# Kernel tuning notes

Measured on AMD Instinct MI355X. Metric: run time of the kernel, lower is better.

The kernel has to match this reference:

```python
import jax, jax.numpy as jnp
import numpy as np

B, S, H, HEADS, STEP = 128, 256, 128, 8, 1


def setup_inputs() -> dict:
    key = jax.random.key(0)
    ks = jax.random.split(key, 20)
    rn = lambda k, shape: jax.random.normal(k, shape, dtype=jnp.float32) * 0.1
    return {
        "A": jax.random.uniform(ks[0], (B, S, 2 * S), dtype=jnp.float32),
        "hidden": jax.random.normal(ks[1], (B, S, H), dtype=jnp.float32),
        "mask": jnp.ones((B, S), dtype=jnp.int32),
        "w_ih": rn(ks[2], (3 * H, 2 * H)),
        "w_hh": rn(ks[3], (3 * H, H)),
        "b_ih": rn(ks[4], (3 * H,)),
        "b_hh": rn(ks[5], (3 * H,)),
        "b_iah": rn(ks[6], (H,)),
        "b_oah": rn(ks[7], (H,)),
        "W_ein": rn(ks[8], (H, H)), "b_ein": rn(ks[9], (H,)),
        "W_eout": rn(ks[10], (H, H)), "b_eout": rn(ks[11], (H,)),
        "W_q0": rn(ks[12], (H, H)), "b_q0": rn(ks[13], (H,)),
        "W_q1": rn(ks[14], (H, H)), "b_q1": rn(ks[15], (H,)),
        "W_q2": rn(ks[16], (H, H)), "b_q2": rn(ks[17], (H,)),
    }


def _forward(A, hidden, mask, w_ih, w_hh, b_ih, b_hh, b_iah, b_oah,
             W_ein, b_ein, W_eout, b_eout, W_q0, b_q0, W_q1, b_q1, W_q2, b_q2):
    b, s, h = hidden.shape
    dk = h // HEADS
    # ---- GNN: gated graph propagation (GRU cell over adjacency messages) ----
    for _ in range(STEP):
        msg_in = A[:, :, :s] @ (hidden @ W_ein.T + b_ein) + b_iah    # [B,S,H]
        msg_out = A[:, :, s:] @ (hidden @ W_eout.T + b_eout) + b_oah  # [B,S,H]
        inputs = jnp.concatenate([msg_in, msg_out], axis=2)           # [B,S,2H]
        gi = inputs @ w_ih.T + b_ih                                   # [B,S,3H]
        gh = hidden @ w_hh.T + b_hh                                   # [B,S,3H]
        i_r, i_i, i_n = jnp.split(gi, 3, axis=2)
        h_r, h_i, h_n = jnp.split(gh, 3, axis=2)
        resetgate = jax.nn.sigmoid(i_r + h_r)
        inputgate = jax.nn.sigmoid(i_i + h_i)
        newgate = jnp.tanh(i_n + resetgate * h_n)
        hidden = hidden - inputgate * (hidden - newgate)
    # ---- query: hidden state of the last valid item in each session ----
    last_idx = jnp.sum(mask, axis=1) - 1
    ht1 = hidden[jnp.arange(b), last_idx]                             # [B,H]
    # ---- LastAttenion: sigmoid score + double softmax readout ----
    q0 = (ht1 @ W_q0.T + b_q0).reshape(b, HEADS, dk)                  # [B,h,dk]
    q1 = (hidden @ W_q1.T + b_q1).reshape(b, s, HEADS, dk).transpose(0, 2, 1, 3)
    q2 = (hidden @ W_q2.T + b_q2).reshape(b, s, HEADS, dk).transpose(0, 2, 1, 3)
    # q0 is expanded over the query axis, so every score row is identical
    alpha = jax.nn.sigmoid(jnp.einsum('bhd,bhjd->bhj', q0, q1))        # [B,h,S]
    alpha = jnp.broadcast_to(alpha[:, :, None, :], (b, HEADS, s, s))   # [B,h,S,S]
    alpha = jax.nn.softmax(alpha, axis=-1)
    row_keep = (mask > 0)[:, None, :, None]                            # [B,1,S,1]
    alpha = jnp.where(row_keep, alpha, -jnp.inf)
    alpha = jax.nn.softmax(2.0 * alpha, axis=1)                        # over heads
    alpha = jnp.where(row_keep, alpha, 0.0)  # guard fully-masked rows (torch would NaN)
    x = jnp.einsum('bhij,bhjd->bhid', alpha, q2)                       # [B,h,S,dk]
    x = x.transpose(0, 2, 1, 3).reshape(b, s, h)                       # [B,S,H]
    a = jnp.sum(x * mask[:, :, None].astype(x.dtype), axis=1)          # [B,H]
    return a


def reference(A, hidden, mask, w_ih, w_hh, b_ih, b_hh, b_iah, b_oah,
              W_ein, b_ein, W_eout, b_eout, W_q0, b_q0, W_q1, b_q1, W_q2, b_q2):
    return _forward(A, hidden, mask, w_ih, w_hh, b_ih, b_hh, b_iah, b_oah,
                    W_ein, b_ein, W_eout, b_eout, W_q0, b_q0, W_q1, b_q1, W_q2, b_q2)
```

## Files before the change

kernel.cpp:

```cpp
#include <hip/hip_runtime.h>
#include <cstdint>
#include <cstddef>

#define BB   128
#define SS   256
#define HH   128
#define NH   8
#define DKK  16

typedef unsigned short u16;
typedef __attribute__((ext_vector_type(8))) short   sh8;
typedef __attribute__((ext_vector_type(4))) float   f32x4;

__device__ __forceinline__ float sigmoidf_(float x) { return 1.f / (1.f + expf(-x)); }

__device__ __forceinline__ u16 f2bf(float x) {
    union { float f; unsigned int u; } v; v.f = x;
    unsigned int r = (v.u + 0x7fffu + ((v.u >> 16) & 1u)) >> 16;
    return (u16)r;
}
__device__ __forceinline__ float bf2f(u16 u) {
    union { unsigned int u; float f; } v; v.u = ((unsigned int)u) << 16;
    return v.f;
}
__device__ __forceinline__ float bflo(unsigned u) {
    union { unsigned u; float f; } v; v.u = u << 16; return v.f;
}
__device__ __forceinline__ float bfhi(unsigned u) {
    union { unsigned u; float f; } v; v.u = u & 0xffff0000u; return v.f;
}

#define BKk 32
#define PK  40

template<int XMODE, int OMODE>
__global__ __launch_bounds__(256) void gemm_mfma(
    const void* __restrict__ Xa, const void* __restrict__ Xc, int ldx, int ldx1, int ksplit,
    long long sXb, long long sXh,
    const u16* __restrict__ Bw, int ldb, long long sBb, long long sBh,
    const float* __restrict__ bias,
    void* __restrict__ Out, long long ldo, long long sOb, long long sOh,
    int K, const u16* __restrict__ hid)
{
    __shared__ __align__(16) char smem[2 * 128 * PK * 2];
    u16* As = (u16*)smem;
    u16* Bs = (u16*)(smem + 128 * PK * 2);

    const int t  = threadIdx.x;
    const int bm = blockIdx.x * 128;
    const int bn = blockIdx.y * 128;
    const long long zb = blockIdx.z >> 1, zh = blockIdx.z & 1;

    const u16* Bp = Bw + zb * sBb + zh * sBh;

    const int wave = t >> 6, lane = t & 63;
    const int wr = (wave >> 1) * 64, wc = (wave & 1) * 64;
    const int fm = lane & 15, fq = lane >> 4;

    f32x4 acc[4][4] = {};

    const int r0  = t >> 2, kk0 = (t & 3) * 8;
    const int r1  = t >> 3, kk1 = (t & 7) * 4;

    uint4  px0, px1, pb0, pb1;
    float4 pf0, pf1, pf2, pf3;

#define LOADX32(K0)                                                                  \
    if (XMODE == 1) {                                                                \
        const float* Xf_ = (const float*)Xa + zb * sXb + zh * sXh;                   \
        const float* xp_ = Xf_ + (long long)(bm + r1) * ldx + (K0) + kk1;            \
        pf0 = *(const float4*)(xp_);                                                 \
        pf1 = *(const float4*)(xp_ + 32LL * ldx);                                    \
        pf2 = *(const float4*)(xp_ + 64LL * ldx);                                    \
        pf3 = *(const float4*)(xp_ + 96LL * ldx);                                    \
    } else if (XMODE == 2 && (K0) >= ksplit) {                                       \
        const u16* xp_ = (const u16*)Xc + (long long)(bm + r0) * ldx1                \
                         + ((K0) - ksplit) + kk0;                                    \
        px0 = *(const uint4*)(xp_);                                                  \
        px1 = *(const uint4*)(xp_ + 64LL * ldx1);                                    \
    } else {                                                                         \
        const u16* xp_ = (const u16*)Xa + (long long)(bm + r0) * ldx + (K0) + kk0;   \
        px0 = *(const uint4*)(xp_);                                                  \
        px1 = *(const uint4*)(xp_ + 64LL * ldx);                                     \
    }

#define LOADB32(K0)                                                                  \
    {                                                                                \
        const u16* bp_ = Bp + (long long)(bn + r0) * ldb + (K0) + kk0;               \
        pb0 = *(const uint4*)(bp_);                                                  \
        pb1 = *(const uint4*)(bp_ + 64LL * ldb);                                     \
    }

    LOADX32(0)
    LOADB32(0)

    for (int k0 = 0; k0 < K; k0 += BKk) {
        if (XMODE == 1) {
            ushort4 w0 = { f2bf(pf0.x), f2bf(pf0.y), f2bf(pf0.z), f2bf(pf0.w) };
            ushort4 w1 = { f2bf(pf1.x), f2bf(pf1.y), f2bf(pf1.z), f2bf(pf1.w) };
            ushort4 w2 = { f2bf(pf2.x), f2bf(pf2.y), f2bf(pf2.z), f2bf(pf2.w) };
            ushort4 w3 = { f2bf(pf3.x), f2bf(pf3.y), f2bf(pf3.z), f2bf(pf3.w) };
            *(ushort4*)&As[(r1     ) * PK + kk1] = w0;
            *(ushort4*)&As[(r1 + 32) * PK + kk1] = w1;
            *(ushort4*)&As[(r1 + 64) * PK + kk1] = w2;
            *(ushort4*)&As[(r1 + 96) * PK + kk1] = w3;
        } else {
            *(uint4*)&As[(r0     ) * PK + kk0] = px0;
            *(uint4*)&As[(r0 + 64) * PK + kk0] = px1;
        }
        *(uint4*)&Bs[(r0     ) * PK + kk0] = pb0;
        *(uint4*)&Bs[(r0 + 64) * PK + kk0] = pb1;
        __syncthreads();

        if (k0 + BKk < K) {
            LOADX32(k0 + BKk)
            LOADB32(k0 + BKk)
        }

        sh8 af[4], bfr[4];
        #pragma unroll
        for (int i = 0; i < 4; i++) af[i]  = *(const sh8*)&As[(wr + i * 16 + fm) * PK + fq * 8];
        #pragma unroll
        for (int j = 0; j < 4; j++) bfr[j] = *(const sh8*)&Bs[(wc + j * 16 + fm) * PK + fq * 8];
        #pragma unroll
        for (int i = 0; i < 4; i++)
            #pragma unroll
            for (int j = 0; j < 4; j++)
                acc[i][j] = __builtin_amdgcn_mfma_f32_16x16x32_bf16(af[i], bfr[j], acc[i][j], 0, 0, 0);
        __syncthreads();
    }
#undef LOADX32
#undef LOADB32

    #pragma unroll
    for (int j = 0; j < 4; j++) {
        const int col = bn + wc + j * 16 + fm;
        const float bj = bias ? bias[col] : 0.f;
        #pragma unroll
        for (int i = 0; i < 4; i++) {
            const int row0 = bm + wr + i * 16 + fq * 4;
            if (OMODE == 1) {
                u16* O = (u16*)Out + zb * sOb + zh * sOh;
                #pragma unroll
                for (int r = 0; r < 4; r++)
                    O[(long long)(row0 + r) * ldo + col] = f2bf(acc[i][j][r] + bj);
            } else {
                u16* O = (u16*)Out + zb * sOb + zh * sOh;
                ushort4 w = { f2bf(acc[i][j][0] + bj), f2bf(acc[i][j][1] + bj),
                              f2bf(acc[i][j][2] + bj), f2bf(acc[i][j][3] + bj) };
                *(ushort4*)&O[(long long)col * ldo + row0] = w;
            }
        }
    }
}

#define BKD  64
#define PKB  72
#define ABUF (128 * PKB)
#define BUFH (2 * ABUF)

template<int XMODE, int OMODE>
__global__ __launch_bounds__(256) void gemm_dbuf(
    const void* __restrict__ Xa, const void* __restrict__ Xc, int ldx, int ldx1, int ksplit,
    long long sXb, long long sXh,
    const u16* __restrict__ Bw, int ldb, long long sBb, long long sBh,
    const float* __restrict__ bias,
    void* __restrict__ Out, long long ldo, long long sOb, long long sOh,
    int K, const u16* __restrict__ hid)
{
    __shared__ __align__(16) char smem[2 * BUFH * 2];
    u16* base = (u16*)smem;

    const int t  = threadIdx.x;
    const int bm = blockIdx.x * 128;
    const int bn = blockIdx.y * 128;
    const long long zb = blockIdx.z >> 1, zh = blockIdx.z & 1;

    const u16* Bp = Bw + zb * sBb + zh * sBh;

    const int wave = t >> 6, lane = t & 63;
    const int wr = (wave >> 1) * 64, wc = (wave & 1) * 64;
    const int fm = lane & 15, fq = lane >> 4;

    f32x4 acc[4][4] = {};

    const int rs = t >> 3, kcs = (t & 7) * 8;

    uint4  px0, px1, px2, px3, pb0, pb1, pb2, pb3;

#define LOADX64(K0)                                                                  \
    if (XMODE == 2 && (K0) >= ksplit) {                                              \
        const u16* xp_ = (const u16*)Xc + (long long)(bm + rs) * ldx1               \
                         + ((K0) - ksplit) + kcs;                                    \
        px0 = *(const uint4*)(xp_);                                                  \
        px1 = *(const uint4*)(xp_ + 32LL * ldx1);                                    \
        px2 = *(const uint4*)(xp_ + 64LL * ldx1);                                    \
        px3 = *(const uint4*)(xp_ + 96LL * ldx1);                                    \
    } else {                                                                         \
        const u16* xp_ = (const u16*)Xa + (long long)(bm + rs) * ldx + (K0) + kcs;   \
        px0 = *(const uint4*)(xp_);                                                  \
        px1 = *(const uint4*)(xp_ + 32LL * ldx);                                     \
        px2 = *(const uint4*)(xp_ + 64LL * ldx);                                     \
        px3 = *(const uint4*)(xp_ + 96LL * ldx);                                     \
    }

#define LOADB64(K0)                                                                  \
    {                                                                                \
        const u16* bp_ = Bp + (long long)(bn + rs) * ldb + (K0) + kcs;               \
        pb0 = *(const uint4*)(bp_);                                                  \
        pb1 = *(const uint4*)(bp_ + 32LL * ldb);                                     \
        pb2 = *(const uint4*)(bp_ + 64LL * ldb);                                     \
        pb3 = *(const uint4*)(bp_ + 96LL * ldb);                                     \
    }

#define COMMIT64(Ad, Bd)                                                             \
    *(uint4*)&(Ad)[(rs     ) * PKB + kcs] = px0;                                     \
    *(uint4*)&(Ad)[(rs + 32) * PKB + kcs] = px1;                                     \
    *(uint4*)&(Ad)[(rs + 64) * PKB + kcs] = px2;                                     \
    *(uint4*)&(Ad)[(rs + 96) * PKB + kcs] = px3;                                     \
    *(uint4*)&(Bd)[(rs     ) * PKB + kcs] = pb0;                                     \
    *(uint4*)&(Bd)[(rs + 32) * PKB + kcs] = pb1;                                     \
    *(uint4*)&(Bd)[(rs + 64) * PKB + kcs] = pb2;                                     \
    *(uint4*)&(Bd)[(rs + 96) * PKB + kcs] = pb3;

    const int nt = K / BKD;
    int cur = 0;

    LOADX64(0)
    LOADB64(0)
    {
        u16* Ad = base;
        u16* Bd = base + ABUF;
        COMMIT64(Ad, Bd)
    }
    __syncthreads();

    for (int tt = 0; tt < nt; ++tt) {
        if (tt + 1 < nt) {
            LOADX64((tt + 1) * BKD)
            LOADB64((tt + 1) * BKD)
        }

        const u16* Ac = base + cur * BUFH;
        const u16* Bc = Ac + ABUF;
        #pragma unroll
        for (int ks = 0; ks < 2; ks++) {
            sh8 af[4], bfr[4];
            #pragma unroll
            for (int i = 0; i < 4; i++)
                af[i]  = *(const sh8*)&Ac[(wr + i * 16 + fm) * PKB + ks * 32 + fq * 8];
            #pragma unroll
            for (int j = 0; j < 4; j++)
                bfr[j] = *(const sh8*)&Bc[(wc + j * 16 + fm) * PKB + ks * 32 + fq * 8];
            #pragma unroll
            for (int i = 0; i < 4; i++)
                #pragma unroll
                for (int j = 0; j < 4; j++)
                    acc[i][j] = __builtin_amdgcn_mfma_f32_16x16x32_bf16(af[i], bfr[j], acc[i][j], 0, 0, 0);
        }

        if (tt + 1 < nt) {
            u16* Ad = base + (cur ^ 1) * BUFH;
            u16* Bd = Ad + ABUF;
            COMMIT64(Ad, Bd)
        }
        __syncthreads();
        cur ^= 1;
    }
#undef LOADX64
#undef LOADB64
#undef COMMIT64

    {
        float* g4s = (float*)smem;
        const int chbase = bn >> 2;
        const int s_t = t >> 3;
        const int cq  = t & 7;
        u16* O = (u16*)Out;
        const int sbase = (wr ? 16 : 0) + fq * 4;
        #pragma unroll
        for (int i = 0; i < 4; i++) {
            #pragma unroll
            for (int j = 0; j < 4; j++) {
                const int q = wc + j * 16 + fm;
                const float bj = bias[bn + q];
                #pragma unroll
                for (int r = 0; r < 4; r++)
                    g4s[(sbase + r) * 132 + q] = acc[i][j][r] + bj;
            }
            __syncthreads();
            {
                const int grow = bm + i * 16 + (s_t < 16 ? s_t : s_t + 48);
                const ushort4 hv = *(const ushort4*)&hid[(long long)grow * HH + chbase + 4 * cq];
                const float hvv[4] = { bf2f(hv.x), bf2f(hv.y), bf2f(hv.z), bf2f(hv.w) };
                ushort4 w;
                u16* wp = (u16*)&w;
                #pragma unroll
                for (int m = 0; m < 4; m++) {
                    f32x4 gv = *(const f32x4*)&g4s[s_t * 132 + 16 * cq + 4 * m];
                    float rg = sigmoidf_(gv[0]);
                    float ig = sigmoidf_(gv[1]);
                    float ng = tanhf(gv[2] + rg * gv[3]);
                    wp[m] = f2bf(hvv[m] - ig * (hvv[m] - ng));
                }
                *(ushort4*)&O[(long long)grow * ldo + chbase + 4 * cq] = w;
            }
            __syncthreads();
        }
    }
}

__global__ __launch_bounds__(256) void k_prepw(
    const float* __restrict__ hidden, u16* __restrict__ h_bf,
    const float* __restrict__ w_ih, const float* __restrict__ w_hh,
    const float* __restrict__ b_ih, const float* __restrict__ b_hh,
    const float* __restrict__ b_iah, const float* __restrict__ b_oah,
    const float* __restrict__ W_ein, const float* __restrict__ b_ein,
    const float* __restrict__ W_eout, const float* __restrict__ b_eout,
    const float* __restrict__ W_q1, const float* __restrict__ b_q1,
    const float* __restrict__ W_q2, const float* __restrict__ b_q2,
    u16* __restrict__ W2bf, float* __restrict__ bias2,
    u16* __restrict__ Wcat, float* __restrict__ biascat,
    u16* __restrict__ Wq12, float* __restrict__ biasq12)
{
    int idx = blockIdx.x * 256 + threadIdx.x;
    {
        float4 v = ((const float4*)hidden)[idx];
        ushort4 w = { f2bf(v.x), f2bf(v.y), f2bf(v.z), f2bf(v.w) };
        ((ushort4*)h_bf)[idx] = w;
    }
    if (idx < 512 * 384) {
        int np = idx / 384, kk = idx % 384;
        int c = np >> 2, g = np & 3;
        float v;
        if (g < 2)       v = (kk < 256) ? w_ih[(g * 128 + c) * 256 + kk]
                                        : w_hh[(g * 128 + c) * 128 + kk - 256];
        else if (g == 2) v = (kk < 256) ? w_ih[(256 + c) * 256 + kk] : 0.f;
        else             v = (kk < 256) ? 0.f : w_hh[(256 + c) * 128 + kk - 256];
        W2bf[idx] = f2bf(v);
    }
    if (idx < 256 * 128) {
        int n = idx >> 7, k = idx & 127;
        Wcat[idx] = f2bf(n < 128 ? W_ein[n * 128 + k] : W_eout[(n - 128) * 128 + k]);
        Wq12[idx] = f2bf(n < 128 ? W_q1[n * 128 + k]  : W_q2[(n - 128) * 128 + k]);
    }
    if (idx < 512) {
        int np = idx, c = np >> 2, g = np & 3;
        float s;
        if (g < 2)       s = b_ih[g * 128 + c] + b_hh[g * 128 + c];
        else if (g == 2) s = b_ih[256 + c];
        else             s = b_hh[256 + c];
        if (g < 3) {
            int n = (g < 2) ? g * 128 + c : 256 + c;
            for (int k = 0; k < 128; k++)
                s += w_ih[n * 256 + k] * b_iah[k] + w_ih[n * 256 + 128 + k] * b_oah[k];
        }
        bias2[np] = s;
    }
    if (idx < 256) {
        biascat[idx] = idx < 128 ? b_ein[idx] : b_eout[idx - 128];
        biasq12[idx] = idx < 128 ? b_q1[idx]  : b_q2[idx - 128];
    }
}

__global__ __launch_bounds__(1024) void k_tail(
    const u16* __restrict__ hnew_bf, const int* __restrict__ mask,
    const u16* __restrict__ q12, const float* __restrict__ Wq0,
    const float* __restrict__ bq0, float* __restrict__ out)
{
    const int b = blockIdx.x, chb = blockIdx.y, t = threadIdx.x;
    __shared__ float red[1024];
    __shared__ float red2[1024][2];
    __shared__ float hs[HH];
    __shared__ float q0s[HH];
    __shared__ float p_s[NH][SS];
    __shared__ float w_s[NH][SS];
    __shared__ int s_nv;

    if (t < 256) {
        int v = mask[b * SS + t];
        #pragma unroll
        for (int m = 1; m < 64; m <<= 1) v += __shfl_xor(v, m, 64);
        if ((t & 63) == 0) red[t >> 6] = (float)v;
    }
    __syncthreads();
    if (t == 0) s_nv = (int)(red[0] + red[1] + red[2] + red[3]);
    __syncthreads();
    const int nv = s_nv;
    const int last = (nv - 1) & (SS - 1);

    if (t < HH) hs[t] = bf2f(hnew_bf[((size_t)b * SS + last) * HH + t]);
    __syncthreads();

    {
        const int n = t & 127, kh = t >> 7;
        const float* w = Wq0 + (size_t)n * HH + kh * 16;
        const float* h = hs + kh * 16;
        float s = 0.f;
        #pragma unroll
        for (int k = 0; k < 16; k++) s += h[k] * w[k];
        red[t] = s;
    }
    __syncthreads();
    if (t < HH) {
        float s = bq0[t];
        #pragma unroll
        for (int kh = 0; kh < 8; kh++) s += red[kh * 128 + t];
        q0s[t] = s;
    }
    __syncthreads();

    {
        const int j = t >> 2, q = t & 3;
        const u16* q1r = q12 + ((size_t)b * SS + j) * 256 + q * 32;
        uint4 va = *(const uint4*)(q1r);
        uint4 vb = *(const uint4*)(q1r + 8);
        uint4 vc = *(const uint4*)(q1r + 16);
        uint4 vd = *(const uint4*)(q1r + 24);
        const float* qa = q0s + q * 32;
        float s0 = qa[0]  * bflo(va.x) + qa[1]  * bfhi(va.x)
                 + qa[2]  * bflo(va.y) + qa[3]  * bfhi(va.y)
                 + qa[4]  * bflo(va.z) + qa[5]  * bfhi(va.z)
                 + qa[6]  * bflo(va.w) + qa[7]  * bfhi(va.w)
                 + qa[8]  * bflo(vb.x) + qa[9]  * bfhi(vb.x)
                 + qa[10] * bflo(vb.y) + qa[11] * bfhi(vb.y)
                 + qa[12] * bflo(vb.z) + qa[13] * bfhi(vb.z)
                 + qa[14] * bflo(vb.w) + qa[15] * bfhi(vb.w);
        float s1 = qa[16] * bflo(vc.x) + qa[17] * bfhi(vc.x)
                 + qa[18] * bflo(vc.y) + qa[19] * bfhi(vc.y)
                 + qa[20] * bflo(vc.z) + qa[21] * bfhi(vc.z)
                 + qa[22] * bflo(vc.w) + qa[23] * bfhi(vc.w)
                 + qa[24] * bflo(vd.x) + qa[25] * bfhi(vd.x)
                 + qa[26] * bflo(vd.y) + qa[27] * bfhi(vd.y)
                 + qa[28] * bflo(vd.z) + qa[29] * bfhi(vd.z)
                 + qa[30] * bflo(vd.w) + qa[31] * bfhi(vd.w);
        p_s[2 * q][j]     = sigmoidf_(s0);
        p_s[2 * q + 1][j] = sigmoidf_(s1);
    }
    __syncthreads();

    if (t < 256) {
        const int h = t >> 5, l = t & 31;
        float v[8], m = -1e30f;
        #pragma unroll
        for (int u = 0; u < 8; u++) { v[u] = p_s[h][l * 8 + u]; m = fmaxf(m, v[u]); }
        #pragma unroll
        for (int msk = 1; msk < 32; msk <<= 1) m = fmaxf(m, __shfl_xor(m, msk, 32));
        float sum = 0.f;
        #pragma unroll
        for (int u = 0; u < 8; u++) { v[u] = expf(v[u] - m); sum += v[u]; }
        #pragma unroll
        for (int msk = 1; msk < 32; msk <<= 1) sum += __shfl_xor(sum, msk, 32);
        const float inv = 1.f / sum;
        #pragma unroll
        for (int u = 0; u < 8; u++) p_s[h][l * 8 + u] = v[u] * inv;
    }
    __syncthreads();

    if (t < 256) {
        float e[NH], den = 0.f;
        #pragma unroll
        for (int h = 0; h < NH; h++) { e[h] = expf(2.f * p_s[h][t]); den += e[h]; }
        const float inv = 1.f / den;
        #pragma unroll
        for (int h = 0; h < NH; h++) w_s[h][t] = e[h] * inv;
    }
    __syncthreads();

    {
        const int cp = t & 31, jq = t >> 5;
        const int col = chb * 64 + cp * 2;
        const int h0 = col >> 4;
        const u16* q2b = q12 + (size_t)b * SS * 256 + 128 + col;
        float a0 = 0.f, a1 = 0.f;
        #pragma unroll
        for (int u = 0; u < 8; u++) {
            const int j = jq * 8 + u;
            const unsigned v = *(const unsigned*)&q2b[(size_t)j * 256];
            const float w = w_s[h0][j];
            a0 += w * bflo(v);
            a1 += w * bfhi(v);
        }
        red2[t][0] = a0;
        red2[t][1] = a1;
    }
    __syncthreads();
    if (t < 64) {
        const int cp2 = t >> 1, par = t & 1;
        float s = 0.f;
        #pragma unroll
        for (int q = 0; q < 32; q++) s += red2[q * 32 + cp2][par];
        out[(size_t)b * HH + chb * 64 + cp2 * 2 + par] = s * (float)nv;
    }
}

extern "C" void kernel_launch(void* const* d_in, const int* in_sizes, int n_in,
                              void* d_out, int out_size, void* d_ws, size_t ws_size,
                              hipStream_t stream)
{
    const float* A      = (const float*)d_in[0];
    const float* hidden = (const float*)d_in[1];
    const int*   mask   = (const int*)d_in[2];
    const float* w_ih   = (const float*)d_in[3];
    const float* w_hh   = (const float*)d_in[4];
    const float* b_ih   = (const float*)d_in[5];
    const float* b_hh   = (const float*)d_in[6];
    const float* b_iah  = (const float*)d_in[7];
    const float* b_oah  = (const float*)d_in[8];
    const float* W_ein  = (const float*)d_in[9];
    const float* b_ein  = (const float*)d_in[10];
    const float* W_eout = (const float*)d_in[11];
    const float* b_eout = (const float*)d_in[12];
    const float* W_q0   = (const float*)d_in[13];
    const float* b_q0   = (const float*)d_in[14];
    const float* W_q1   = (const float*)d_in[15];
    const float* b_q1   = (const float*)d_in[16];
    const float* W_q2   = (const float*)d_in[17];
    const float* b_q2   = (const float*)d_in[18];
    float* out = (float*)d_out;
    char* ws = (char*)d_ws;

    u16*   Et      = (u16*)(ws + 0);
    u16*   Mbuf    = (u16*)(ws + 16777216);
    u16*   q12bf   = (u16*)(ws + 0);
    u16*   hnew_bf = (u16*)(ws + 33554432);
    u16*   h_bf    = (u16*)(ws + 41943040);
    u16*   W2bf    = (u16*)(ws + 50331648);
    u16*   Wcat    = (u16*)(ws + 50724864);
    u16*   Wq12    = (u16*)(ws + 50790400);
    float* bias2   = (float*)(ws + 50855936);
    float* biascat = (float*)(ws + 50857984);
    float* biasq12 = (float*)(ws + 50859008);

    k_prepw<<<4096, 256, 0, stream>>>(hidden, h_bf,
                                      w_ih, w_hh, b_ih, b_hh, b_iah, b_oah,
                                      W_ein, b_ein, W_eout, b_eout,
                                      W_q1, b_q1, W_q2, b_q2,
                                      W2bf, bias2, Wcat, biascat, Wq12, biasq12);

    gemm_mfma<0, 2><<<dim3(256, 2, 1), 256, 0, stream>>>(
        h_bf, nullptr, HH, 0, 0, 0, 0,
        Wcat, HH, 0, 0, biascat,
        Et, 32768, 0, 0, HH, nullptr);

    gemm_mfma<1, 1><<<dim3(2, 1, 256), 256, 0, stream>>>(
        A, nullptr, 512, 0, 0, 131072LL, 256LL,
        Et, 32768, 256LL, 128LL * 32768LL, nullptr,
        Mbuf, 256, 65536LL, 128LL, SS, nullptr);

    gemm_dbuf<2, 3><<<dim3(256, 4, 1), 256, 0, stream>>>(
        Mbuf, h_bf, 256, HH, 256, 0, 0,
        W2bf, 384, 0, 0, bias2,
        hnew_bf, HH, 0, 0, 384, h_bf);

    gemm_mfma<0, 1><<<dim3(256, 2, 1), 256, 0, stream>>>(
        hnew_bf, nullptr, HH, 0, 0, 0, 0,
        Wq12, HH, 0, 0, biasq12,
        q12bf, 256, 0, 0, HH, nullptr);

    k_tail<<<dim3(BB, 2), 1024, 0, stream>>>(hnew_bf, mask, q12bf, W_q0, b_q0, out);
}
```

Measured before the change: 215.3 us.

## Fuse q1/q2 projection GEMM into tail kernel using in-LDS MFMA

Removes the separate q12 projection GEMM launch and instead computes q1 (all 128 cols) and the needed half of q2 per block inside k_tail with bf16 MFMA from hidden and weights staged in shared memory. This avoids writing and re-reading the q12 intermediate through global memory and one kernel launch. In exchange, q1 is recomputed by both column-half blocks, and the tail kernel now uses about 148KB of LDS, which limits it to one block per CU. It also drops some unused batched-stride code from the GEMM kernels.

```diff
diff --git a/kernel.cpp b/kernel.cpp
--- a/kernel.cpp
+++ b/kernel.cpp
@@ -73,11 +73,6 @@
         pf1 = *(const float4*)(xp_ + 32LL * ldx);                                    \
         pf2 = *(const float4*)(xp_ + 64LL * ldx);                                    \
         pf3 = *(const float4*)(xp_ + 96LL * ldx);                                    \
-    } else if (XMODE == 2 && (K0) >= ksplit) {                                       \
-        const u16* xp_ = (const u16*)Xc + (long long)(bm + r0) * ldx1                \
-                         + ((K0) - ksplit) + kk0;                                    \
-        px0 = *(const uint4*)(xp_);                                                  \
-        px1 = *(const uint4*)(xp_ + 64LL * ldx1);                                    \
     } else {                                                                         \
         const u16* xp_ = (const u16*)Xa + (long long)(bm + r0) * ldx + (K0) + kk0;   \
         px0 = *(const uint4*)(xp_);                                                  \
@@ -174,9 +169,8 @@
     const int t  = threadIdx.x;
     const int bm = blockIdx.x * 128;
     const int bn = blockIdx.y * 128;
-    const long long zb = blockIdx.z >> 1, zh = blockIdx.z & 1;
-
-    const u16* Bp = Bw + zb * sBb + zh * sBh;
+
+    const u16* Bp = Bw;
 
     const int wave = t >> 6, lane = t & 63;
     const int wr = (wave >> 1) * 64, wc = (wave & 1) * 64;
@@ -363,19 +357,99 @@
     }
 }
 
+#define HP 136
+#define QP 72
+
 __global__ __launch_bounds__(1024) void k_tail(
     const u16* __restrict__ hnew_bf, const int* __restrict__ mask,
-    const u16* __restrict__ q12, const float* __restrict__ Wq0,
-    const float* __restrict__ bq0, float* __restrict__ out)
+    const u16* __restrict__ Wq12, const float* __restrict__ biasq12,
+    const float* __restrict__ Wq0, const float* __restrict__ bq0,
+    float* __restrict__ out)
 {
+    __shared__ __align__(16) char smem[151560];
+    u16*   Hs   = (u16*)smem;
+    u16*   Wst  = (u16*)(smem + 69632);
+    u16*   q1s  = (u16*)smem;
+    u16*   q2s  = (u16*)(smem + 69632);
+    float* red  = (float*)(smem + 121856);
+    float* red2 = (float*)(smem + 125952);
+    float* p_s  = (float*)(smem + 134144);
+    float* w_s  = (float*)(smem + 142336);
+    float* hs   = (float*)(smem + 150528);
+    float* q0s  = (float*)(smem + 151040);
+    int*   s_nv = (int*)(smem + 151552);
+
     const int b = blockIdx.x, chb = blockIdx.y, t = threadIdx.x;
-    __shared__ float red[1024];
-    __shared__ float red2[1024][2];
-    __shared__ float hs[HH];
-    __shared__ float q0s[HH];
-    __shared__ float p_s[NH][SS];
-    __shared__ float w_s[NH][SS];
-    __shared__ int s_nv;
+    const int wave = t >> 6, lane = t & 63;
+    const int fm = lane & 15, fq = lane >> 4;
+    const int wrow = (wave >> 2) * 64;
+    const int wc1  = (wave & 3) * 32;
+    const int wc2  = (wave & 3) * 16;
+
+    {
+        const int row = t >> 2, kc = (t & 3) * 32;
+        const u16* hp = hnew_bf + ((size_t)b * SS + row) * HH + kc;
+        uint4 v0 = *(const uint4*)(hp);
+        uint4 v1 = *(const uint4*)(hp + 8);
+        uint4 v2 = *(const uint4*)(hp + 16);
+        uint4 v3 = *(const uint4*)(hp + 24);
+        *(uint4*)&Hs[row * HP + kc     ] = v0;
+        *(uint4*)&Hs[row * HP + kc + 8 ] = v1;
+        *(uint4*)&Hs[row * HP + kc + 16] = v2;
+        *(uint4*)&Hs[row * HP + kc + 24] = v3;
+    }
+    if (t < 768) {
+        const int row = t >> 2, kc = (t & 3) * 32;
+        const int gr = (row < 128) ? row : 128 + chb * 64 + (row - 128);
+        const u16* wp = Wq12 + (size_t)gr * HH + kc;
+        uint4 v0 = *(const uint4*)(wp);
+        uint4 v1 = *(const uint4*)(wp + 8);
+        uint4 v2 = *(const uint4*)(wp + 16);
+        uint4 v3 = *(const uint4*)(wp + 24);
+        *(uint4*)&Wst[row * HP + kc     ] = v0;
+        *(uint4*)&Wst[row * HP + kc + 8 ] = v1;
+        *(uint4*)&Wst[row * HP + kc + 16] = v2;
+        *(uint4*)&Wst[row * HP + kc + 24] = v3;
+    }
+    __syncthreads();
+
+    f32x4 a1[4][2] = {};
+    f32x4 a2[4] = {};
+    #pragma unroll
+    for (int ks = 0; ks < 4; ks++) {
+        sh8 af[4], b1[2], b2;
+        #pragma unroll
+        for (int i = 0; i < 4; i++)
+            af[i] = *(const sh8*)&Hs[(wrow + i * 16 + fm) * HP + ks * 32 + fq * 8];
+        #pragma unroll
+        for (int j = 0; j < 2; j++)
+            b1[j] = *(const sh8*)&Wst[(wc1 + j * 16 + fm) * HP + ks * 32 + fq * 8];
+        b2 = *(const sh8*)&Wst[(128 + wc2 + fm) * HP + ks * 32 + fq * 8];
+        #pragma unroll
+        for (int i = 0; i < 4; i++) {
+            #pragma unroll
+            for (int j = 0; j < 2; j++)
+                a1[i][j] = __builtin_amdgcn_mfma_f32_16x16x32_bf16(af[i], b1[j], a1[i][j], 0, 0, 0);
+            a2[i] = __builtin_amdgcn_mfma_f32_16x16x32_bf16(af[i], b2, a2[i], 0, 0, 0);
+        }
+    }
+    __syncthreads();
+
+    {
+        const float bq1a = biasq12[wc1 + fm];
+        const float bq1b = biasq12[wc1 + 16 + fm];
+        const float bq2  = biasq12[128 + chb * 64 + wc2 + fm];
+        #pragma unroll
+        for (int i = 0; i < 4; i++)
+            #pragma unroll
+            for (int r = 0; r < 4; r++) {
+                const int row = wrow + i * 16 + fq * 4 + r;
+                q1s[row * HP + wc1 + fm]      = f2bf(a1[i][0][r] + bq1a);
+                q1s[row * HP + wc1 + 16 + fm] = f2bf(a1[i][1][r] + bq1b);
+                q2s[row * QP + wc2 + fm]      = f2bf(a2[i][r] + bq2);
+            }
+    }
+    __syncthreads();
 
     if (t < 256) {
         int v = mask[b * SS + t];
@@ -384,9 +458,9 @@
         if ((t & 63) == 0) red[t >> 6] = (float)v;
     }
     __syncthreads();
-    if (t == 0) s_nv = (int)(red[0] + red[1] + red[2] + red[3]);
-    __syncthreads();
-    const int nv = s_nv;
+    if (t == 0) *s_nv = (int)(red[0] + red[1] + red[2] + red[3]);
+    __syncthreads();
+    const int nv = *s_nv;
     const int last = (nv - 1) & (SS - 1);
 
     if (t < HH) hs[t] = bf2f(hnew_bf[((size_t)b * SS + last) * HH + t]);
@@ -412,7 +486,7 @@
 
     {
         const int j = t >> 2, q = t & 3;
-        const u16* q1r = q12 + ((size_t)b * SS + j) * 256 + q * 32;
+        const u16* q1r = q1s + j * HP + q * 32;
         uint4 va = *(const uint4*)(q1r);
         uint4 vb = *(const uint4*)(q1r + 8);
         uint4 vc = *(const uint4*)(q1r + 16);
@@ -434,8 +508,8 @@
                  + qa[26] * bflo(vd.y) + qa[27] * bfhi(vd.y)
                  + qa[28] * bflo(vd.z) + qa[29] * bfhi(vd.z)
                  + qa[30] * bflo(vd.w) + qa[31] * bfhi(vd.w);
-        p_s[2 * q][j]     = sigmoidf_(s0);
-        p_s[2 * q + 1][j] = sigmoidf_(s1);
+        p_s[(2 * q) * SS + j]     = sigmoidf_(s0);
+        p_s[(2 * q + 1) * SS + j] = sigmoidf_(s1);
     }
     __syncthreads();
 
@@ -443,7 +517,7 @@
         const int h = t >> 5, l = t & 31;
         float v[8], m = -1e30f;
         #pragma unroll
-        for (int u = 0; u < 8; u++) { v[u] = p_s[h][l * 8 + u]; m = fmaxf(m, v[u]); }
+        for (int u = 0; u < 8; u++) { v[u] = p_s[h * SS + l * 8 + u]; m = fmaxf(m, v[u]); }
         #pragma unroll
         for (int msk = 1; msk < 32; msk <<= 1) m = fmaxf(m, __shfl_xor(m, msk, 32));
         float sum = 0.f;
@@ -453,17 +527,17 @@
         for (int msk = 1; msk < 32; msk <<= 1) sum += __shfl_xor(sum, msk, 32);
         const float inv = 1.f / sum;
         #pragma unroll
-        for (int u = 0; u < 8; u++) p_s[h][l * 8 + u] = v[u] * inv;
+        for (int u = 0; u < 8; u++) p_s[h * SS + l * 8 + u] = v[u] * inv;
     }
     __syncthreads();
 
     if (t < 256) {
         float e[NH], den = 0.f;
         #pragma unroll
-        for (int h = 0; h < NH; h++) { e[h] = expf(2.f * p_s[h][t]); den += e[h]; }
+        for (int h = 0; h < NH; h++) { e[h] = expf(2.f * p_s[h * SS + t]); den += e[h]; }
         const float inv = 1.f / den;
         #pragma unroll
-        for (int h = 0; h < NH; h++) w_s[h][t] = e[h] * inv;
+        for (int h = 0; h < NH; h++) w_s[h * SS + t] = e[h] * inv;
     }
     __syncthreads();
 
@@ -471,25 +545,24 @@
         const int cp = t & 31, jq = t >> 5;
         const int col = chb * 64 + cp * 2;
         const int h0 = col >> 4;
-        const u16* q2b = q12 + (size_t)b * SS * 256 + 128 + col;
-        float a0 = 0.f, a1 = 0.f;
+        float a0 = 0.f, a1v = 0.f;
         #pragma unroll
         for (int u = 0; u < 8; u++) {
             const int j = jq * 8 + u;
-            const unsigned v = *(const unsigned*)&q2b[(size_t)j * 256];
-            const float w = w_s[h0][j];
-            a0 += w * bflo(v);
-            a1 += w * bfhi(v);
-        }
-        red2[t][0] = a0;
-        red2[t][1] = a1;
+            const unsigned v = *(const unsigned*)&q2s[j * QP + cp * 2];
+            const float w = w_s[h0 * SS + j];
+            a0  += w * bflo(v);
+            a1v += w * bfhi(v);
+        }
+        red2[t * 2 + 0] = a0;
+        red2[t * 2 + 1] = a1v;
     }
     __syncthreads();
     if (t < 64) {
         const int cp2 = t >> 1, par = t & 1;
         float s = 0.f;
         #pragma unroll
-        for (int q = 0; q < 32; q++) s += red2[q * 32 + cp2][par];
+        for (int q = 0; q < 32; q++) s += red2[(q * 32 + cp2) * 2 + par];
         out[(size_t)b * HH + chb * 64 + cp2 * 2 + par] = s * (float)nv;
     }
 }
@@ -522,7 +595,6 @@
 
     u16*   Et      = (u16*)(ws + 0);
     u16*   Mbuf    = (u16*)(ws + 16777216);
-    u16*   q12bf   = (u16*)(ws + 0);
     u16*   hnew_bf = (u16*)(ws + 33554432);
     u16*   h_bf    = (u16*)(ws + 41943040);
     u16*   W2bf    = (u16*)(ws + 50331648);
@@ -553,10 +625,6 @@
         W2bf, 384, 0, 0, bias2,
         hnew_bf, HH, 0, 0, 384, h_bf);
 
-    gemm_mfma<0, 1><<<dim3(256, 2, 1), 256, 0, stream>>>(
-        hnew_bf, nullptr, HH, 0, 0, 0, 0,
-        Wq12, HH, 0, 0, biasq12,
-        q12bf, 256, 0, 0, HH, nullptr);
-
-    k_tail<<<dim3(BB, 2), 1024, 0, stream>>>(hnew_bf, mask, q12bf, W_q0, b_q0, out);
-}
+    k_tail<<<dim3(BB, 2), 1024, 0, stream>>>(hnew_bf, mask, Wq12, biasq12,
+                                             W_q0, b_q0, out);
+}
```

Result: faster. 208.4 us (-3.2%).
